# Kernel optimization log

Hardware: AMD Instinct MI355X
Metric: run time of the kernel (lower is better)

The kernel has to match this reference:

```python
import jax, jax.numpy as jnp
import numpy as np

# ---- fixed pillar-encoder config (matches init_kwargs) ----
PC_MIN = np.array([-51.2, -51.2, -5.0], dtype=np.float32)
PC_MAX = np.array([51.2, 51.2, 3.0], dtype=np.float32)
VOXEL = np.array([0.2, 0.2, 8.0], dtype=np.float32)
BEV_W = int(round((PC_MAX[0] - PC_MIN[0]) / VOXEL[0]))  # 512
BEV_H = int(round((PC_MAX[1] - PC_MIN[1]) / VOXEL[1]))  # 512
SCALE_XY = BEV_W * BEV_H
SCALE_X = BEV_W
BN_EPS = 1e-3
N_PTS = 400_000
N_BEV_FEAT = 64


def setup_inputs() -> dict:
    key = jax.random.key(0)
    ks = jax.random.split(key, 8)
    B = 2
    b_idx = jax.random.randint(ks[0], (N_PTS,), 0, B).astype(jnp.float32)
    xy = jax.random.uniform(ks[1], (N_PTS, 2), minval=-51.0, maxval=51.0)
    z = jax.random.uniform(ks[2], (N_PTS, 1), minval=-4.9, maxval=2.9)
    intensity = jax.random.uniform(ks[3], (N_PTS, 1))
    t = jax.random.uniform(ks[4], (N_PTS, 1))
    points = jnp.concatenate([b_idx[:, None], xy, z, intensity, t], axis=1)  # (N, 6)
    W = jax.random.normal(ks[5], (10, N_BEV_FEAT), dtype=jnp.float32) * 0.05
    bn_gamma = jax.random.uniform(ks[6], (N_BEV_FEAT,), minval=0.5, maxval=1.5)
    bn_beta = jax.random.normal(ks[7], (N_BEV_FEAT,), dtype=jnp.float32) * 0.1
    bn_mean = jnp.zeros((N_BEV_FEAT,), jnp.float32)
    bn_var = jnp.ones((N_BEV_FEAT,), jnp.float32)
    return {"points": points, "W": W, "bn_gamma": bn_gamma, "bn_beta": bn_beta,
            "bn_mean": bn_mean, "bn_var": bn_var, "batch_size": B}


def reference(points, W, bn_gamma, bn_beta, bn_mean, bn_var, batch_size):
    pc_min = jnp.asarray(PC_MIN)
    voxel = jnp.asarray(VOXEL)
    xyz = points[:, 1:4]
    xy = points[:, 1:3]

    # ---- pillarize ----
    bev_coord = jnp.floor((xy - pc_min[:2]) / voxel[:2]).astype(jnp.int32)  # (N, 2) [x, y]
    b_idx = points[:, 0].astype(jnp.int32)
    flat = b_idx * SCALE_XY + bev_coord[:, 1] * SCALE_X + bev_coord[:, 0]  # (N,)
    num_seg = batch_size * SCALE_XY

    # scatter_mean over pillars (dense segment form == unique-based scatter_mean)
    sums = jax.ops.segment_sum(xyz, flat, num_segments=num_seg)            # (P, 3)
    cnt = jax.ops.segment_sum(jnp.ones((xyz.shape[0], 1), xyz.dtype), flat, num_segments=num_seg)
    mean = sums / jnp.maximum(cnt, 1.0)
    f_mean = xyz - mean[flat]                                              # (N, 3)
    xy_offset = voxel[:2] / 2.0 + pc_min[:2]
    f_center = xy - (bev_coord.astype(xy.dtype) * voxel[:2] + xy_offset)   # (N, 2)
    feat = jnp.concatenate([points[:, 1:6], f_mean, f_center], axis=1)     # (N, 10)

    # ---- pointnet: Linear(no bias) + BN1d(eval) + ReLU ----
    h = feat @ W
    h = (h - bn_mean) * jax.lax.rsqrt(bn_var + BN_EPS) * bn_gamma + bn_beta
    h = jax.nn.relu(h)                                                     # (N, C)

    # ---- scatter_max into dense BEV (empty pillars -> 0) ----
    pill = jax.ops.segment_max(h, flat, num_segments=num_seg)
    bev = jnp.where(cnt > 0, pill, 0.0)
    bev_img = bev.reshape(batch_size, BEV_H, BEV_W, h.shape[1])            # (B, H, W, C)

    # ---- per-point bilinear interpolation of BEV features ----
    px = (points[:, 1] - pc_min[0]) / voxel[0]
    py = (points[:, 2] - pc_min[1]) / voxel[1]
    x0 = jnp.clip(jnp.floor(px).astype(jnp.int32), 0, BEV_W - 1)
    x1 = jnp.clip(jnp.floor(px).astype(jnp.int32) + 1, 0, BEV_W - 1)
    y0 = jnp.clip(jnp.floor(py).astype(jnp.int32), 0, BEV_H - 1)
    y1 = jnp.clip(jnp.floor(py).astype(jnp.int32) + 1, 0, BEV_H - 1)
    Ia = bev_img[b_idx, y0, x0]
    Ib = bev_img[b_idx, y1, x0]
    Ic = bev_img[b_idx, y0, x1]
    Id = bev_img[b_idx, y1, x1]
    wa = (x1.astype(px.dtype) - px) * (y1.astype(py.dtype) - py)
    wb = (x1.astype(px.dtype) - px) * (py - y0.astype(py.dtype))
    wc = (px - x0.astype(px.dtype)) * (y1.astype(py.dtype) - py)
    wd = (px - x0.astype(px.dtype)) * (py - y0.astype(py.dtype))
    points_feat = Ia * wa[:, None] + Ib * wb[:, None] + Ic * wc[:, None] + Id * wd[:, None]
    return points_feat  # (N, C)
```

## Files before the change

kernel.cpp:

```cpp
#include <hip/hip_runtime.h>

#define BEV_W    512
#define BEV_H    512
#define SCALE_XY (BEV_W * BEV_H)
#define NPTS     400000
#define NFEAT    64
#define BATCH    2
#define NSEG     (BATCH * SCALE_XY)

#define SUMS_BYTES ((size_t)NSEG * sizeof(unsigned long long))
#define BEV_FLOATS ((size_t)NSEG * 64)

#define XY_SCALE 2048.0f
#define XY_INV   (1.0f / 2048.0f)
#define XY_BIAS  131072
#define Z_SCALE  256.0f
#define Z_INV    (1.0f / 256.0f)
#define Z_BIAS   2048

__device__ __forceinline__ float coordf(float v) {
    return (v + 51.2f) * 5.0f;
}
__device__ __forceinline__ int vox_coord(float v) {
    return (int)floorf(coordf(v));
}

__global__ void __launch_bounds__(256)
kA_scatter_sums(const float* __restrict__ pts,
                unsigned long long* __restrict__ sumsc) {
    int p = blockIdx.x * blockDim.x + threadIdx.x;
    if (p >= NPTS) return;
    const float* pp = pts + (size_t)p * 6;
    float b = pp[0], x = pp[1], y = pp[2], z = pp[3];
    int cx = vox_coord(x);
    int cy = vox_coord(y);
    int flat = (int)b * SCALE_XY + cy * BEV_W + cx;
    unsigned long long ex = (unsigned int)(__float2int_rn(x * XY_SCALE) + XY_BIAS);
    unsigned long long ey = (unsigned int)(__float2int_rn(y * XY_SCALE) + XY_BIAS);
    unsigned long long ez = (unsigned int)(__float2int_rn(z * Z_SCALE) + Z_BIAS);
    unsigned long long u = ex | (ey << 22) | (ez << 44) | (1ull << 60);
    atomicAdd(&sumsc[flat], u);
}

#define KB_K 8
__global__ void __launch_bounds__(256)
kB_pillar_max(const float* __restrict__ pts, const float* __restrict__ Wm,
              const float* __restrict__ gamma, const float* __restrict__ beta,
              const float* __restrict__ bmean, const float* __restrict__ bvar,
              const unsigned long long* __restrict__ sumsc,
              unsigned int* __restrict__ bev) {
    __shared__ float sW[10 * 64];
    __shared__ float sScale[64];
    __shared__ float sShift[64];
    int tid = threadIdx.x;
    for (int i = tid; i < 640; i += 256) sW[i] = Wm[i];
    if (tid < 64) {
        float sc = gamma[tid] * rsqrtf(bvar[tid] + 0.001f);
        sScale[tid] = sc;
        sShift[tid] = beta[tid] - bmean[tid] * sc;
    }
    __syncthreads();

    int wid  = tid >> 6;
    int lane = tid & 63;
    int p0 = (blockIdx.x * 4 + wid) * KB_K;
    p0 = __builtin_amdgcn_readfirstlane(p0);
    if (p0 >= NPTS) return;

    float rec[6 * KB_K];
    const float* pbase = pts + (size_t)p0 * 6;
    #pragma unroll
    for (int i = 0; i < 6 * KB_K; ++i) rec[i] = pbase[i];

    int                flats[KB_K];
    unsigned long long uv[KB_K];
    #pragma unroll
    for (int k = 0; k < KB_K; ++k) {
        float x = rec[6 * k + 1], y = rec[6 * k + 2];
        int b  = (int)rec[6 * k + 0];
        int cx = vox_coord(x);
        int cy = vox_coord(y);
        int fl = b * SCALE_XY + cy * BEV_W + cx;
        fl = __builtin_amdgcn_readfirstlane(fl);
        flats[k] = fl;
        uv[k] = sumsc[fl];
    }

    const float XOFF = 0.1f + -51.2f;
    int j = lane;
    #pragma unroll
    for (int k = 0; k < KB_K; ++k) {
        float x = rec[6 * k + 1], y = rec[6 * k + 2], z = rec[6 * k + 3];
        float it = rec[6 * k + 4], tt = rec[6 * k + 5];
        int cx = vox_coord(x);
        int cy = vox_coord(y);

        unsigned long long u = uv[k];
        int n = (int)(u >> 60);
        long long sx = (long long)(u & 0x3FFFFFULL)         - (long long)n * XY_BIAS;
        long long sy = (long long)((u >> 22) & 0x3FFFFFULL) - (long long)n * XY_BIAS;
        long long sz = (long long)((u >> 44) & 0xFFFFULL)   - (long long)n * Z_BIAS;
        float c = fmaxf((float)n, 1.0f);
        float inv = __builtin_amdgcn_rcpf(c);
        float mx = ((float)sx * XY_INV) * inv;
        float my = ((float)sy * XY_INV) * inv;
        float mz = ((float)sz * Z_INV) * inv;

        float fcx = x - ((float)cx * 0.2f + XOFF);
        float fcy = y - ((float)cy * 0.2f + XOFF);

        float h = x  * sW[0 * 64 + j]
                + y  * sW[1 * 64 + j]
                + z  * sW[2 * 64 + j]
                + it * sW[3 * 64 + j]
                + tt * sW[4 * 64 + j]
                + (x - mx) * sW[5 * 64 + j]
                + (y - my) * sW[6 * 64 + j]
                + (z - mz) * sW[7 * 64 + j]
                + fcx * sW[8 * 64 + j]
                + fcy * sW[9 * 64 + j];

        h = h * sScale[j] + sShift[j];
        h = fmaxf(h, 0.0f);

        if (n == 1) {
            bev[(size_t)flats[k] * 64 + j] = __float_as_uint(h);
        } else if (h > 0.0f) {
            atomicMax((int*)(bev + (size_t)flats[k] * 64 + j), __float_as_int(h));
        }
    }
}

#define KC_K 4
__global__ void __launch_bounds__(256)
kC_bilinear(const float* __restrict__ pts, const float* __restrict__ bev,
            float* __restrict__ out) {
    int tid  = threadIdx.x;
    int wid  = tid >> 6;
    int lane = tid & 63;
    int p0 = (blockIdx.x * 4 + wid) * KC_K;
    p0 = __builtin_amdgcn_readfirstlane(p0);
    if (p0 >= NPTS) return;

    float rec[6 * KC_K];
    const float* pbase = pts + (size_t)p0 * 6;
    #pragma unroll
    for (int i = 0; i < 6 * KC_K; ++i) rec[i] = pbase[i];

    float Ia[KC_K], Ib[KC_K], Ic[KC_K], Id[KC_K];
    float wa[KC_K], wb[KC_K], wc[KC_K], wd[KC_K];
    #pragma unroll
    for (int k = 0; k < KC_K; ++k) {
        float x = rec[6 * k + 1], y = rec[6 * k + 2];
        int b = (int)rec[6 * k + 0];
        float px = coordf(x);
        float py = coordf(y);
        int fx = (int)floorf(px);
        int fy = (int)floorf(py);
        int x0 = min(max(fx, 0), BEV_W - 1);
        int x1 = min(max(fx + 1, 0), BEV_W - 1);
        int y0 = min(max(fy, 0), BEV_H - 1);
        int y1 = min(max(fy + 1, 0), BEV_H - 1);

        wa[k] = ((float)x1 - px) * ((float)y1 - py);
        wb[k] = ((float)x1 - px) * (py - (float)y0);
        wc[k] = (px - (float)x0) * ((float)y1 - py);
        wd[k] = (px - (float)x0) * (py - (float)y0);

        size_t base = (size_t)b * SCALE_XY * 64 + lane;
        Ia[k] = bev[base + (size_t)(y0 * BEV_W + x0) * 64];
        Ib[k] = bev[base + (size_t)(y1 * BEV_W + x0) * 64];
        Ic[k] = bev[base + (size_t)(y0 * BEV_W + x1) * 64];
        Id[k] = bev[base + (size_t)(y1 * BEV_W + x1) * 64];
    }

    #pragma unroll
    for (int k = 0; k < KC_K; ++k) {
        float v = Ia[k] * wa[k] + Ib[k] * wb[k] + Ic[k] * wc[k] + Id[k] * wd[k];
        __builtin_nontemporal_store(v, &out[(size_t)(p0 + k) * 64 + lane]);
    }
}

extern "C" void kernel_launch(void* const* d_in, const int* in_sizes, int n_in,
                              void* d_out, int out_size, void* d_ws, size_t ws_size,
                              hipStream_t stream) {
    const float* pts   = (const float*)d_in[0];
    const float* Wm    = (const float*)d_in[1];
    const float* gamma = (const float*)d_in[2];
    const float* beta  = (const float*)d_in[3];
    const float* bmean = (const float*)d_in[4];
    const float* bvar  = (const float*)d_in[5];
    float* out = (float*)d_out;

    unsigned long long* sumsc = (unsigned long long*)d_ws;
    unsigned int* bev = (unsigned int*)((char*)d_ws + SUMS_BYTES);

    (void)hipMemsetAsync(d_ws, 0, SUMS_BYTES + BEV_FLOATS * sizeof(float), stream);

    kA_scatter_sums<<<(NPTS + 255) / 256, 256, 0, stream>>>(pts, sumsc);
    kB_pillar_max<<<NPTS / (4 * KB_K), 256, 0, stream>>>(pts, Wm, gamma, beta,
                                                         bmean, bvar, sumsc, bev);
    kC_bilinear<<<NPTS / (4 * KC_K), 256, 0, stream>>>(pts, (const float*)bev, out);
}
```

Measured before the change: 165.1 us.

## Zero only occupied BEV pillars in scatter kernel and mask empty cells on read

Drops the full-size memset of the dense BEV feature buffer and instead has each point zero its own pillar's 64-float row during the sum-scatter kernel. The bilinear kernel then reads each neighbour's point count from the packed sums and treats empty pillars as zero, since their rows are never initialized. This removes a large bulk memory clear but adds redundant scattered writes for pillars with multiple points and extra count loads in the interpolation kernel.

```diff
diff --git a/kernel.cpp b/kernel.cpp
--- a/kernel.cpp
+++ b/kernel.cpp
@@ -9,7 +9,6 @@
 #define NSEG     (BATCH * SCALE_XY)
 
 #define SUMS_BYTES ((size_t)NSEG * sizeof(unsigned long long))
-#define BEV_FLOATS ((size_t)NSEG * 64)
 
 #define XY_SCALE 2048.0f
 #define XY_INV   (1.0f / 2048.0f)
@@ -27,7 +26,8 @@
 
 __global__ void __launch_bounds__(256)
 kA_scatter_sums(const float* __restrict__ pts,
-                unsigned long long* __restrict__ sumsc) {
+                unsigned long long* __restrict__ sumsc,
+                float4* __restrict__ bev4) {
     int p = blockIdx.x * blockDim.x + threadIdx.x;
     if (p >= NPTS) return;
     const float* pp = pts + (size_t)p * 6;
@@ -35,6 +35,12 @@
     int cx = vox_coord(x);
     int cy = vox_coord(y);
     int flat = (int)b * SCALE_XY + cy * BEV_W + cx;
+
+    float4 z4 = make_float4(0.f, 0.f, 0.f, 0.f);
+    float4* dst = bev4 + (size_t)flat * 16;
+    #pragma unroll
+    for (int i = 0; i < 16; ++i) dst[i] = z4;
+
     unsigned long long ex = (unsigned int)(__float2int_rn(x * XY_SCALE) + XY_BIAS);
     unsigned long long ey = (unsigned int)(__float2int_rn(y * XY_SCALE) + XY_BIAS);
     unsigned long long ez = (unsigned int)(__float2int_rn(z * Z_SCALE) + Z_BIAS);
@@ -134,6 +140,7 @@
 #define KC_K 4
 __global__ void __launch_bounds__(256)
 kC_bilinear(const float* __restrict__ pts, const float* __restrict__ bev,
+            const unsigned int* __restrict__ sums32,
             float* __restrict__ out) {
     int tid  = threadIdx.x;
     int wid  = tid >> 6;
@@ -148,6 +155,7 @@
     for (int i = 0; i < 6 * KC_K; ++i) rec[i] = pbase[i];
 
     float Ia[KC_K], Ib[KC_K], Ic[KC_K], Id[KC_K];
+    unsigned int ca[KC_K], cb[KC_K], cc[KC_K], cd[KC_K];
     float wa[KC_K], wb[KC_K], wc[KC_K], wd[KC_K];
     #pragma unroll
     for (int k = 0; k < KC_K; ++k) {
@@ -167,16 +175,29 @@
         wc[k] = (px - (float)x0) * ((float)y1 - py);
         wd[k] = (px - (float)x0) * (py - (float)y0);
 
-        size_t base = (size_t)b * SCALE_XY * 64 + lane;
-        Ia[k] = bev[base + (size_t)(y0 * BEV_W + x0) * 64];
-        Ib[k] = bev[base + (size_t)(y1 * BEV_W + x0) * 64];
-        Ic[k] = bev[base + (size_t)(y0 * BEV_W + x1) * 64];
-        Id[k] = bev[base + (size_t)(y1 * BEV_W + x1) * 64];
+        int fA = b * SCALE_XY + y0 * BEV_W + x0;
+        int fB = b * SCALE_XY + y1 * BEV_W + x0;
+        int fC = b * SCALE_XY + y0 * BEV_W + x1;
+        int fD = b * SCALE_XY + y1 * BEV_W + x1;
+
+        ca[k] = sums32[(size_t)fA * 2 + 1] >> 28;
+        cb[k] = sums32[(size_t)fB * 2 + 1] >> 28;
+        cc[k] = sums32[(size_t)fC * 2 + 1] >> 28;
+        cd[k] = sums32[(size_t)fD * 2 + 1] >> 28;
+
+        Ia[k] = bev[(size_t)fA * 64 + lane];
+        Ib[k] = bev[(size_t)fB * 64 + lane];
+        Ic[k] = bev[(size_t)fC * 64 + lane];
+        Id[k] = bev[(size_t)fD * 64 + lane];
     }
 
     #pragma unroll
     for (int k = 0; k < KC_K; ++k) {
-        float v = Ia[k] * wa[k] + Ib[k] * wb[k] + Ic[k] * wc[k] + Id[k] * wd[k];
+        float A = ca[k] ? Ia[k] : 0.0f;
+        float B = cb[k] ? Ib[k] : 0.0f;
+        float C = cc[k] ? Ic[k] : 0.0f;
+        float D = cd[k] ? Id[k] : 0.0f;
+        float v = A * wa[k] + B * wb[k] + C * wc[k] + D * wd[k];
         __builtin_nontemporal_store(v, &out[(size_t)(p0 + k) * 64 + lane]);
     }
 }
@@ -193,12 +214,16 @@
     float* out = (float*)d_out;
 
     unsigned long long* sumsc = (unsigned long long*)d_ws;
-    unsigned int* bev = (unsigned int*)((char*)d_ws + SUMS_BYTES);
-
-    (void)hipMemsetAsync(d_ws, 0, SUMS_BYTES + BEV_FLOATS * sizeof(float), stream);
-
-    kA_scatter_sums<<<(NPTS + 255) / 256, 256, 0, stream>>>(pts, sumsc);
+    float* bev = (float*)((char*)d_ws + SUMS_BYTES);
+
+    (void)hipMemsetAsync(d_ws, 0, SUMS_BYTES, stream);
+
+    kA_scatter_sums<<<(NPTS + 255) / 256, 256, 0, stream>>>(pts, sumsc,
+                                                            (float4*)bev);
     kB_pillar_max<<<NPTS / (4 * KB_K), 256, 0, stream>>>(pts, Wm, gamma, beta,
-                                                         bmean, bvar, sumsc, bev);
-    kC_bilinear<<<NPTS / (4 * KC_K), 256, 0, stream>>>(pts, (const float*)bev, out);
-}
+                                                         bmean, bvar, sumsc,
+                                                         (unsigned int*)bev);
+    kC_bilinear<<<NPTS / (4 * KC_K), 256, 0, stream>>>(pts, (const float*)bev,
+                                                       (const unsigned int*)sumsc,
+                                                       out);
+}
```

New measurement: 182.6 us. +10.6%, slower.
